# Optimization experiments

Measured on AMD Instinct MI355X. Metric: run time of the kernel, lower is better.

Reference implementation:

```python
import jax, jax.numpy as jnp
import numpy as np

N_VERTICES = 500_000
N_EDGES = 16_000_000


def setup_inputs() -> dict:
    key = jax.random.key(0)
    k1, k2, k3 = jax.random.split(key, 3)
    # positive features keep A_ii and the scatter-sum denominator away from zero
    vertex_attr = jax.random.uniform(k1, (N_VERTICES, 2), dtype=jnp.float32, minval=0.1, maxval=1.1)
    edge_attr = jax.random.uniform(k2, (N_EDGES, 3), dtype=jnp.float32, minval=0.1, maxval=1.1)
    edgeij_pair = jax.random.randint(k3, (2, N_EDGES), 0, N_VERTICES, dtype=jnp.int32)
    return {"vertex_attr": vertex_attr, "edge_attr": edge_attr, "edgeij_pair": edgeij_pair}


def reference(vertex_attr, edge_attr, edgeij_pair):
    src = edgeij_pair[0]  # i (row) in PyG MetaLayer convention
    n_vertices = vertex_attr.shape[0]

    A_ij = edge_attr[:, 0]
    S_ij = edge_attr[:, 1]
    v_ij = edge_attr[:, 2]
    # (Layer1_EdgeUpdate appends w_ij = C_j as a 4th edge column, but that
    #  column is never read downstream, so it is omitted here.)

    # Layer1 vertex update: gammabar_i = sum_k A_ik / sum_k A_ik*S_ik*v_ik
    numerator = jax.ops.segment_sum(A_ij, src, num_segments=n_vertices)
    denominator = jax.ops.segment_sum(A_ij * S_ij * v_ij, src, num_segments=n_vertices)
    gammabar = numerator / denominator  # [N]

    A_ii = vertex_attr[:, 0]
    C_i = vertex_attr[:, 1]
    alpha = gammabar / A_ii  # [N]

    # Layer2 edge update: w_ij = (1 - C_i) * (-A_ij * alpha_i), i = src
    w_ij = (1.0 - C_i[src]) * (-A_ij * alpha[src])  # [E]
    return w_ij
```

## Files before the change

kernel.cpp:

```cpp
#include <hip/hip_runtime.h>


#define BINS 256
#define VSHIFT 11
#define VPB 2048
#define NBLK 1024
#define BT 256
#define SBT 512
#define SUB 2048
#define SPLIT 8

#define SC_A 524288.0f
#define SC_D 4194304.0f
#define INV_SCD (1.0f / 4194304.0f)

typedef unsigned int u32;
typedef unsigned short u16;
typedef unsigned char u8;
typedef unsigned long long u64;

static __device__ __forceinline__ u32 f2h(float x) {
    _Float16 h = (_Float16)x; u16 u; __builtin_memcpy(&u, &h, 2); return (u32)u;
}
static __device__ __forceinline__ float h2f(u32 u) {
    u16 v = (u16)u; _Float16 h; __builtin_memcpy(&h, &v, 2); return (float)h;
}


__global__ void hist_k(const int* __restrict__ src, int ne, int chunk,
                       u32* __restrict__ bh) {
    __shared__ u32 h[BINS];
    for (int j = threadIdx.x; j < BINS; j += SBT) h[j] = 0;
    __syncthreads();
    int lo = blockIdx.x * chunk;
    int hi = min(ne, lo + chunk);
    int n = hi - lo;
    int ngroups = (n + 3) >> 2;
    for (int g = threadIdx.x; g < ngroups; g += SBT) {
        int i = lo + (g << 2);
        if (i + 3 < hi) {
            int4 s = *reinterpret_cast<const int4*>(src + i);
            atomicAdd(&h[((u32)s.x) >> VSHIFT], 1u);
            atomicAdd(&h[((u32)s.y) >> VSHIFT], 1u);
            atomicAdd(&h[((u32)s.z) >> VSHIFT], 1u);
            atomicAdd(&h[((u32)s.w) >> VSHIFT], 1u);
        } else {
            for (int j = i; j < hi; ++j)
                atomicAdd(&h[((u32)src[j]) >> VSHIFT], 1u);
        }
    }
    __syncthreads();
    for (int j = threadIdx.x; j < BINS; j += SBT)
        bh[(size_t)blockIdx.x * BINS + j] = h[j];
}

__global__ void scan_col_k(u32* __restrict__ bh, u32* __restrict__ bin_total) {
    const int IT = NBLK / BT;
    int bin = blockIdx.x, t = threadIdx.x;
    u32 v[IT];
    u32 tsum = 0;
    #pragma unroll
    for (int k = 0; k < IT; ++k) {
        v[k] = bh[(size_t)(IT * t + k) * BINS + bin];
        tsum += v[k];
    }
    int lane = t & 63, wv = t >> 6;
    u32 inc = tsum;
    #pragma unroll
    for (int d = 1; d < 64; d <<= 1) {
        u32 y = __shfl_up(inc, d);
        if (lane >= d) inc += y;
    }
    __shared__ u32 wsum[BT / 64];
    if (lane == 63) wsum[wv] = inc;
    __syncthreads();
    u32 wbase = 0;
    for (int w = 0; w < wv; ++w) wbase += wsum[w];
    u32 run = wbase + inc - tsum;
    #pragma unroll
    for (int k = 0; k < IT; ++k) {
        u32 c = v[k];
        bh[(size_t)(IT * t + k) * BINS + bin] = run;
        run += c;
    }
    if (t == BT - 1) bin_total[bin] = run;
}

__global__ void scan_bins_k(const u32* __restrict__ bin_total,
                            u32* __restrict__ bin_base) {
    int t = threadIdx.x;
    u32 a0 = (t < BINS) ? bin_total[t] : 0;
    int lane = t & 63, wv = t >> 6;
    u32 inc = a0;
    #pragma unroll
    for (int d = 1; d < 64; d <<= 1) {
        u32 y = __shfl_up(inc, d);
        if (lane >= d) inc += y;
    }
    __shared__ u32 wsum[BT / 64];
    if (lane == 63) wsum[wv] = inc;
    __syncthreads();
    u32 wbase = 0;
    for (int w = 0; w < wv; ++w) wbase += wsum[w];
    if (t < BINS) bin_base[t] = wbase + inc - a0;
    if (t == BINS - 1) bin_base[BINS] = wbase + inc;
}

__global__ __launch_bounds__(SBT, 2)
void scatter_k(const float* __restrict__ eattr,
               const int* __restrict__ src,
               const u32* __restrict__ bh,
               const u32* __restrict__ bin_base,
               uint2* __restrict__ rec,
               u16* __restrict__ ah,
               int ne, int chunk) {
    __shared__ u32 cur[BINS];
    __shared__ u32 lbase[BINS];
    __shared__ u32 loff[BINS];
    __shared__ u32 wsum[SBT / 64];
    __shared__ uint2 stage[SUB];
    __shared__ u8 sbin[SUB];
    int t = threadIdx.x;
    int lane = t & 63, wid = t >> 6;
    for (int j = t; j < BINS; j += SBT)
        cur[j] = bin_base[j] + bh[(size_t)blockIdx.x * BINS + j];
    int lo = blockIdx.x * chunk;
    int hi = min(ne, lo + chunk);
    for (int base = lo; base < hi; base += SUB) {
        int n = min(SUB, hi - base);
        if (t < BINS) lbase[t] = 0;
        __syncthreads();
        uint2 pay[4];
        u8 pb[4];
        {
            int o = t << 2;
            int i = base + o;
            if (o + 3 < n) {
                int4 sv = *reinterpret_cast<const int4*>(src + i);
                const float4* ea = reinterpret_cast<const float4*>(eattr + 3ll * i);
                float4 w0 = ea[0], w1 = ea[1], w2 = ea[2];
                float A[4] = {w0.x, w0.w, w1.z, w2.y};
                float D[4] = {w0.x * w0.y * w0.z, w0.w * w1.x * w1.y,
                              w1.z * w1.w * w2.x, w2.y * w2.z * w2.w};
                int S[4] = {sv.x, sv.y, sv.z, sv.w};
                ushort4 hv;
                u16* hp = &hv.x;
                #pragma unroll
                for (int j = 0; j < 4; ++j) {
                    u32 s = (u32)S[j];
                    u32 ni = __float2uint_rn(A[j] * SC_A);
                    u32 di = __float2uint_rn(D[j] * SC_D);
                    u8 b = (u8)(s >> VSHIFT);
                    pay[j] = make_uint2(di, (ni << VSHIFT) | (s & (VPB - 1)));
                    pb[j] = b;
                    hp[j] = (u16)f2h(A[j]);
                    atomicAdd(&lbase[b], 1u);
                }
                *reinterpret_cast<ushort4*>(ah + i) = hv;
            } else {
                #pragma unroll
                for (int j = 0; j < 4; ++j) {
                    int o2 = o + j;
                    if (o2 < n) {
                        int i2 = base + o2;
                        u32 s = (u32)src[i2];
                        float a  = eattr[3ll * i2];
                        float s1 = eattr[3ll * i2 + 1];
                        float v1 = eattr[3ll * i2 + 2];
                        u32 ni = __float2uint_rn(a * SC_A);
                        u32 di = __float2uint_rn(a * s1 * v1 * SC_D);
                        u8 b = (u8)(s >> VSHIFT);
                        pay[j] = make_uint2(di, (ni << VSHIFT) | (s & (VPB - 1)));
                        pb[j] = b;
                        ah[i2] = (u16)f2h(a);
                        atomicAdd(&lbase[b], 1u);
                    }
                }
            }
        }
        __syncthreads();
        u32 a0 = (t < BINS) ? lbase[t] : 0;
        u32 inc = a0;
        #pragma unroll
        for (int d = 1; d < 64; d <<= 1) {
            u32 y = __shfl_up(inc, d);
            if (lane >= d) inc += y;
        }
        if (lane == 63) wsum[wid] = inc;
        __syncthreads();
        u32 wb = 0;
        for (int w = 0; w < wid; ++w) wb += wsum[w];
        u32 ex = wb + inc - a0;
        if (t < BINS) { lbase[t] = ex; loff[t] = ex; }
        __syncthreads();
        #pragma unroll
        for (int k = 0; k < 4; ++k) {
            int o = (t << 2) + k;
            if (o < n) {
                u8 b = pb[k];
                u32 p = atomicAdd(&loff[b], 1u);
                stage[p] = pay[k];
                sbin[p] = b;
            }
        }
        __syncthreads();
        for (int p = t; p < n; p += SBT) {
            u32 b = sbin[p];
            rec[cur[b] + (u32)p - lbase[b]] = stage[p];
        }
        __syncthreads();
        for (int j = t; j < BINS; j += SBT) cur[j] += loff[j] - lbase[j];
        __syncthreads();
    }
}

__global__ void accum_part_k(const uint2* __restrict__ rec,
                             const u32* __restrict__ bin_base,
                             u64* __restrict__ partial) {
    __shared__ u64 acc[VPB];
    int bin = blockIdx.x / SPLIT;
    int q   = blockIdx.x % SPLIT;
    for (int l = threadIdx.x; l < VPB; l += BT) acc[l] = 0ull;
    __syncthreads();
    u32 s0 = bin_base[bin], s1 = bin_base[bin + 1];
    u32 cnt = s1 - s0;
    u32 ra = s0 + (u32)((u64)cnt * q / SPLIT);
    u32 rb = s0 + (u32)((u64)cnt * (q + 1) / SPLIT);
    for (u32 r = ra + threadIdx.x; r < rb; r += BT) {
        uint2 qq = rec[r];
        u64 add = ((u64)(qq.y >> VSHIFT) << 35) | (u64)qq.x;
        atomicAdd(&acc[qq.y & (VPB - 1)], add);
    }
    __syncthreads();
    u64* po = partial + (size_t)blockIdx.x * VPB;
    for (int l = threadIdx.x; l < VPB; l += BT) po[l] = acc[l];
}

__global__ void coef_part_k(const u64* __restrict__ partial,
                            const float* __restrict__ vattr,
                            float* __restrict__ coef, int nv) {
    int v = blockIdx.x * blockDim.x + threadIdx.x;
    int stride = gridDim.x * blockDim.x;
    for (; v < nv; v += stride) {
        int bin = v >> VSHIFT, l = v & (VPB - 1);
        size_t base = ((size_t)bin * SPLIT << VSHIFT) + l;
        float num = 0.f, den = 0.f;
        #pragma unroll
        for (int sp = 0; sp < SPLIT; ++sp) {
            u64 p = partial[base + ((size_t)sp << VSHIFT)];
            num += (float)(u32)(p >> 32);
            den += (float)(u32)p;
        }
        float2 va = reinterpret_cast<const float2*>(vattr)[v];
        float gam = num / den;
        coef[v] = (1.0f - va.y) * (-gam / va.x);
    }
}


#define FPSCALE 8388608.0f
#define FPINV   (1.0f / 8388608.0f)

__global__ void zero_u64(u64* __restrict__ p, int n) {
    int i = blockIdx.x * blockDim.x + threadIdx.x;
    int stride = gridDim.x * blockDim.x;
    for (; i < n; i += stride) p[i] = 0ull;
}

__global__ void accum_packed(const float* __restrict__ eattr,
                             const int* __restrict__ src,
                             u64* __restrict__ accp,
                             u16* __restrict__ ah, int ne) {
    int t = blockIdx.x * blockDim.x + threadIdx.x;
    int stride = gridDim.x * blockDim.x;
    for (int i = t; i < ne; i += stride) {
        float a = eattr[3ll * i];
        float d = a * eattr[3ll * i + 1] * eattr[3ll * i + 2];
        u32 ni = (u32)__float2uint_rn(a * FPSCALE);
        u32 di = (u32)__float2uint_rn(d * FPSCALE);
        atomicAdd(&accp[(u32)src[i]], ((u64)ni << 32) | (u64)di);
        if (ah) ah[i] = (u16)f2h(a);
    }
}

__global__ void coef_packed(const float* __restrict__ vattr,
                            const u64* __restrict__ accp,
                            float* __restrict__ coef, int nv) {
    int v = blockIdx.x * blockDim.x + threadIdx.x;
    int stride = gridDim.x * blockDim.x;
    for (; v < nv; v += stride) {
        u64 a = accp[v];
        float num = (float)(u32)(a >> 32) * FPINV;
        float den = (float)(u32)a * FPINV;
        float2 va = reinterpret_cast<const float2*>(vattr)[v];
        coef[v] = (1.0f - va.y) * (-(num / den) / va.x);
    }
}


__global__ void finalize(const u16* __restrict__ ah,
                         const float* __restrict__ edge_attr,
                         const int* __restrict__ src,
                         const float* __restrict__ coef,
                         float* __restrict__ out, int ne4, int n_edges) {
    int t = blockIdx.x * blockDim.x + threadIdx.x;
    int stride = gridDim.x * blockDim.x;
    for (int i = t; i < ne4; i += stride) {
        int4 s = reinterpret_cast<const int4*>(src)[i];
        float4 A;
        if (ah) {
            ushort4 h = reinterpret_cast<const ushort4*>(ah)[i];
            A.x = h2f(h.x); A.y = h2f(h.y); A.z = h2f(h.z); A.w = h2f(h.w);
        } else {
            const float* e = edge_attr + 12ll * i;
            A.x = e[0]; A.y = e[3]; A.z = e[6]; A.w = e[9];
        }
        float4 w;
        w.x = coef[s.x] * A.x;
        w.y = coef[s.y] * A.y;
        w.z = coef[s.z] * A.z;
        w.w = coef[s.w] * A.w;
        reinterpret_cast<float4*>(out)[i] = w;
    }
    for (int e = 4 * ne4 + t; e < n_edges; e += stride) {
        float Ae = ah ? h2f(ah[e]) : edge_attr[3ll * e];
        out[e] = coef[src[e]] * Ae;
    }
}

extern "C" void kernel_launch(void* const* d_in, const int* in_sizes, int n_in,
                              void* d_out, int out_size, void* d_ws, size_t ws_size,
                              hipStream_t stream) {
    const float* vattr = (const float*)d_in[0];
    const float* eattr = (const float*)d_in[1];
    const int*   pair  = (const int*)d_in[2];
    int nv = in_sizes[0] / 2;
    int ne = in_sizes[1] / 3;
    const int* src = pair;
    float* out = (float*)d_out;

    int ne4 = ne / 4;
    auto capped = [](long long want, int cap) {
        return (int)(want < cap ? (want > 1 ? want : 1) : cap);
    };
    int fgrid = capped(((long long)ne4 + BT - 1) / BT, 4096);

    size_t off = 0;
    float* coef = (float*)((char*)d_ws + off); off += (size_t)nv * 4;
    off = (off + 255) & ~(size_t)255;
    u32* bin_total = (u32*)((char*)d_ws + off); off += (size_t)BINS * 4;
    u32* bin_base  = (u32*)((char*)d_ws + off); off += (size_t)(BINS + 1) * 4;
    off = (off + 255) & ~(size_t)255;
    u32* bh  = (u32*)((char*)d_ws + off); off += (size_t)NBLK * BINS * 4;
    off = (off + 255) & ~(size_t)255;
    u64* partial = (u64*)((char*)d_ws + off); off += ((size_t)BINS * SPLIT << VSHIFT) * 8;
    off = (off + 255) & ~(size_t)255;
    uint2* rec = (uint2*)((char*)d_ws + off); off += 8ull * ne;
    off = (off + 255) & ~(size_t)255;
    u16* ah = (u16*)((char*)d_ws + off); off += 2ull * ne;
    long long chunk_ll = ((((long long)ne + NBLK - 1) / NBLK) + SUB - 1) / SUB * SUB;
    bool main_ok = ws_size >= off && nv <= (BINS << VSHIFT) &&
                   chunk_ll * NBLK < 2147000000ll;
    int chunk = (int)chunk_ll;

    if (main_ok) {
        hist_k<<<NBLK, SBT, 0, stream>>>(src, ne, chunk, bh);
        scan_col_k<<<BINS, BT, 0, stream>>>(bh, bin_total);
        scan_bins_k<<<1, BT, 0, stream>>>(bin_total, bin_base);
        scatter_k<<<NBLK, SBT, 0, stream>>>(eattr, src, bh, bin_base, rec, ah, ne, chunk);
        accum_part_k<<<BINS * SPLIT, BT, 0, stream>>>(rec, bin_base, partial);
        coef_part_k<<<capped(((long long)nv + BT - 1) / BT, 2048), BT, 0, stream>>>(partial, vattr, coef, nv);
        finalize<<<fgrid, BT, 0, stream>>>(ah, eattr, src, coef, out, ne4, ne);
    } else {
        u64* accp = (u64*)d_ws;
        float* fcoef = (float*)(accp + nv);
        size_t fb_base = (size_t)nv * 12;
        fb_base = (fb_base + 255) & ~(size_t)255;
        u16* fah = nullptr;
        if (ws_size >= fb_base + 2ull * ne)
            fah = (u16*)((char*)d_ws + fb_base);
        int zgrid = capped(((long long)nv + BT - 1) / BT, 2048);
        int agrid = capped(((long long)ne + BT - 1) / BT, 4096);
        int cgrid = capped(((long long)nv + BT - 1) / BT, 2048);
        zero_u64<<<zgrid, BT, 0, stream>>>(accp, nv);
        accum_packed<<<agrid, BT, 0, stream>>>(eattr, src, accp, fah, ne);
        coef_packed<<<cgrid, BT, 0, stream>>>(vattr, accp, fcoef, nv);
        finalize<<<fgrid, BT, 0, stream>>>(fah, eattr, src, fcoef, out, ne4, ne);
    }
}
```

Baseline: 274.6 us.

## Replace scatter prefix-scan staging with capped per-bin slots and prefetch next tile

```diff
diff --git a/kernel.cpp b/kernel.cpp
--- a/kernel.cpp
+++ b/kernel.cpp
@@ -9,14 +9,13 @@
 #define SBT 512
 #define SUB 2048
 #define SPLIT 8
+#define CAP 16
 
 #define SC_A 524288.0f
 #define SC_D 4194304.0f
-#define INV_SCD (1.0f / 4194304.0f)
 
 typedef unsigned int u32;
 typedef unsigned short u16;
-typedef unsigned char u8;
 typedef unsigned long long u64;
 
 static __device__ __forceinline__ u32 f2h(float x) {
@@ -115,102 +114,93 @@
                u16* __restrict__ ah,
                int ne, int chunk) {
     __shared__ u32 cur[BINS];
-    __shared__ u32 lbase[BINS];
-    __shared__ u32 loff[BINS];
-    __shared__ u32 wsum[SBT / 64];
-    __shared__ uint2 stage[SUB];
-    __shared__ u8 sbin[SUB];
+    __shared__ u32 cnt[BINS];
+    __shared__ uint2 stage[BINS * CAP];
     int t = threadIdx.x;
-    int lane = t & 63, wid = t >> 6;
+    int lo = blockIdx.x * chunk;
+    int hi = min(ne, lo + chunk);
+    if (lo >= hi) return;
     for (int j = t; j < BINS; j += SBT)
         cur[j] = bin_base[j] + bh[(size_t)blockIdx.x * BINS + j];
-    int lo = blockIdx.x * chunk;
-    int hi = min(ne, lo + chunk);
-    for (int base = lo; base < hi; base += SUB) {
-        int n = min(SUB, hi - base);
-        if (t < BINS) lbase[t] = 0;
-        __syncthreads();
-        uint2 pay[4];
-        u8 pb[4];
-        {
-            int o = t << 2;
-            int i = base + o;
-            if (o + 3 < n) {
-                int4 sv = *reinterpret_cast<const int4*>(src + i);
-                const float4* ea = reinterpret_cast<const float4*>(eattr + 3ll * i);
-                float4 w0 = ea[0], w1 = ea[1], w2 = ea[2];
-                float A[4] = {w0.x, w0.w, w1.z, w2.y};
-                float D[4] = {w0.x * w0.y * w0.z, w0.w * w1.x * w1.y,
-                              w1.z * w1.w * w2.x, w2.y * w2.z * w2.w};
-                int S[4] = {sv.x, sv.y, sv.z, sv.w};
-                ushort4 hv;
-                u16* hp = &hv.x;
-                #pragma unroll
-                for (int j = 0; j < 4; ++j) {
-                    u32 s = (u32)S[j];
-                    u32 ni = __float2uint_rn(A[j] * SC_A);
-                    u32 di = __float2uint_rn(D[j] * SC_D);
-                    u8 b = (u8)(s >> VSHIFT);
-                    pay[j] = make_uint2(di, (ni << VSHIFT) | (s & (VPB - 1)));
-                    pb[j] = b;
-                    hp[j] = (u16)f2h(A[j]);
-                    atomicAdd(&lbase[b], 1u);
-                }
-                *reinterpret_cast<ushort4*>(ah + i) = hv;
-            } else {
-                #pragma unroll
-                for (int j = 0; j < 4; ++j) {
-                    int o2 = o + j;
-                    if (o2 < n) {
-                        int i2 = base + o2;
-                        u32 s = (u32)src[i2];
-                        float a  = eattr[3ll * i2];
-                        float s1 = eattr[3ll * i2 + 1];
-                        float v1 = eattr[3ll * i2 + 2];
-                        u32 ni = __float2uint_rn(a * SC_A);
-                        u32 di = __float2uint_rn(a * s1 * v1 * SC_D);
-                        u8 b = (u8)(s >> VSHIFT);
-                        pay[j] = make_uint2(di, (ni << VSHIFT) | (s & (VPB - 1)));
-                        pb[j] = b;
-                        ah[i2] = (u16)f2h(a);
-                        atomicAdd(&lbase[b], 1u);
-                    }
+
+    float erA[12], erB[12];
+    int srA[4], srB[4];
+
+    auto LOADV = [&](int base, float* er, int* sr) {
+        int o = t << 2;
+        int n = min(hi - base, SUB);
+        int i = base + o;
+        if (o + 3 < n) {
+            int4 s4 = *reinterpret_cast<const int4*>(src + i);
+            sr[0] = s4.x; sr[1] = s4.y; sr[2] = s4.z; sr[3] = s4.w;
+            const float4* ea = reinterpret_cast<const float4*>(eattr + 3ll * i);
+            float4 w0 = ea[0], w1 = ea[1], w2 = ea[2];
+            er[0] = w0.x; er[1] = w0.y; er[2]  = w0.z; er[3]  = w0.w;
+            er[4] = w1.x; er[5] = w1.y; er[6]  = w1.z; er[7]  = w1.w;
+            er[8] = w2.x; er[9] = w2.y; er[10] = w2.z; er[11] = w2.w;
+        } else {
+            #pragma unroll
+            for (int j = 0; j < 4; ++j) {
+                if (o + j < n) {
+                    sr[j] = src[i + j];
+                    er[3 * j]     = eattr[3ll * (i + j)];
+                    er[3 * j + 1] = eattr[3ll * (i + j) + 1];
+                    er[3 * j + 2] = eattr[3ll * (i + j) + 2];
                 }
             }
         }
+    };
+
+    auto PLACE = [&](int base, float* er, int* sr) {
+        int o = t << 2;
+        int n = min(hi - base, SUB);
+        ushort4 hv;
+        u16* hp = &hv.x;
+        #pragma unroll
+        for (int j = 0; j < 4; ++j) {
+            if (o + j < n) {
+                u32 s = (u32)sr[j];
+                float a = er[3 * j];
+                float d = a * er[3 * j + 1] * er[3 * j + 2];
+                u32 ni = __float2uint_rn(a * SC_A);
+                u32 di = __float2uint_rn(d * SC_D);
+                u32 b = s >> VSHIFT;
+                uint2 pay = make_uint2(di, (ni << VSHIFT) | (s & (VPB - 1)));
+                hp[j] = (u16)f2h(a);
+                u32 slot = atomicAdd(&cnt[b], 1u);
+                if (slot < CAP) stage[(b << 4) | slot] = pay;
+                else rec[cur[b] + slot] = pay;
+            }
+        }
+        if (o + 3 < n) {
+            *reinterpret_cast<ushort4*>(ah + base + o) = hv;
+        } else {
+            #pragma unroll
+            for (int j = 0; j < 4; ++j)
+                if (o + j < n) ah[base + o + j] = hp[j];
+        }
+    };
+
+    LOADV(lo, erA, srA);
+    for (int base = lo; base < hi; base += SUB) {
+        if (t < BINS) cnt[t] = 0;
         __syncthreads();
-        u32 a0 = (t < BINS) ? lbase[t] : 0;
-        u32 inc = a0;
-        #pragma unroll
-        for (int d = 1; d < 64; d <<= 1) {
-            u32 y = __shfl_up(inc, d);
-            if (lane >= d) inc += y;
-        }
-        if (lane == 63) wsum[wid] = inc;
+        PLACE(base, erA, srA);
+        if (base + SUB < hi) LOADV(base + SUB, erB, srB);
         __syncthreads();
-        u32 wb = 0;
-        for (int w = 0; w < wid; ++w) wb += wsum[w];
-        u32 ex = wb + inc - a0;
-        if (t < BINS) { lbase[t] = ex; loff[t] = ex; }
+        #pragma unroll
+        for (int r = 0; r < (BINS * CAP) / SBT; ++r) {
+            int j = t + r * SBT;
+            u32 b = (u32)j >> 4, s = (u32)j & 15u;
+            u32 c = cnt[b];
+            if (s < min(c, (u32)CAP)) rec[cur[b] + s] = stage[j];
+        }
         __syncthreads();
-        #pragma unroll
-        for (int k = 0; k < 4; ++k) {
-            int o = (t << 2) + k;
-            if (o < n) {
-                u8 b = pb[k];
-                u32 p = atomicAdd(&loff[b], 1u);
-                stage[p] = pay[k];
-                sbin[p] = b;
-            }
-        }
-        __syncthreads();
-        for (int p = t; p < n; p += SBT) {
-            u32 b = sbin[p];
-            rec[cur[b] + (u32)p - lbase[b]] = stage[p];
-        }
-        __syncthreads();
-        for (int j = t; j < BINS; j += SBT) cur[j] += loff[j] - lbase[j];
-        __syncthreads();
+        if (t < BINS) cur[t] += cnt[t];
+        #pragma unroll
+        for (int j = 0; j < 12; ++j) erA[j] = erB[j];
+        #pragma unroll
+        for (int j = 0; j < 4; ++j) srA[j] = srB[j];
     }
 }
 
```

Result: slower. 280.3 us (+2.1%).
